# Optimization experiments

Measured on AMD Instinct MI355X. Metric: run time of the kernel, lower is better.

## Reference

```python
import jax, jax.numpy as jnp
import numpy as np

IN_DIM = 64
OUT_DIM = 64


def setup_inputs() -> dict:
    key = jax.random.key(0)
    k1, k2, k3, k4, k5, k6 = jax.random.split(key, 6)
    N, E = 50000, 800000
    features = jax.random.normal(k1, (N, IN_DIM), dtype=jnp.float32)
    src_idx = jax.random.randint(k2, (E,), 0, N, dtype=jnp.int64)
    # torch nn.Linear-style init (uniform +/- 1/sqrt(fan_in)); stored as [in, out]
    s1 = 1.0 / np.sqrt(IN_DIM)
    s2 = 1.0 / np.sqrt(OUT_DIM)
    W1 = jax.random.uniform(k3, (IN_DIM, OUT_DIM), jnp.float32, -s1, s1)
    b1 = jax.random.uniform(k4, (OUT_DIM,), jnp.float32, -s1, s1)
    W2 = jax.random.uniform(k5, (OUT_DIM, OUT_DIM), jnp.float32, -s2, s2)
    b2 = jax.random.uniform(k6, (OUT_DIM,), jnp.float32, -s2, s2)
    return {"features": features, "src_idx": src_idx, "W1": W1, "b1": b1, "W2": W2, "b2": b2}


def reference(features, src_idx, W1, b1, W2, b2):
    # gather source-node features per edge: [E, in_dim]
    x = features[src_idx]
    # Linear -> ReLU -> Linear -> ReLU
    h = jax.nn.relu(x @ W1 + b1)
    out = jax.nn.relu(h @ W2 + b2)  # [E, out_dim] == 'feature_n'
    return out
```

## Files before the change

kernel.cpp:

```cpp
#include <hip/hip_runtime.h>

typedef float f32x4 __attribute__((ext_vector_type(4)));
typedef _Float16 f16;
typedef f16 f16x8 __attribute__((ext_vector_type(8)));


__global__ __launch_bounds__(256) void cvt_kernel(
    const f32x4* __restrict__ in, f16x8* __restrict__ outv, int n8)
{
    const int stride = gridDim.x * blockDim.x;
    for (int i = blockIdx.x * blockDim.x + threadIdx.x; i < n8; i += stride) {
        const f32x4 a = in[2 * i];
        const f32x4 b = in[2 * i + 1];
        f16x8 o;
        #pragma unroll
        for (int j = 0; j < 4; ++j) { o[j] = (f16)a[j]; o[4 + j] = (f16)b[j]; }
        outv[i] = o;
    }
}

__global__ __launch_bounds__(256) void fused_mlp_kernel(
    const f16* __restrict__ feat16,
    const int* __restrict__ src,
    const float* __restrict__ W1, const float* __restrict__ b1,
    const float* __restrict__ W2, const float* __restrict__ b2,
    float* __restrict__ out, int E, int ntiles)
{
    __shared__ f16  hl[4][16][72];
    __shared__ float ol[4][16][68];

    const int lane = threadIdx.x & 63;
    const int wv   = threadIdx.x >> 6;
    const int l15  = lane & 15;
    const int q    = lane >> 4;

    const int gw = blockIdx.x * 4 + wv;
    const int nw = gridDim.x * 4;

    f16x8 B1f[4][2], B2f[4][2];
    #pragma unroll
    for (int t = 0; t < 4; ++t) {
        #pragma unroll
        for (int s = 0; s < 2; ++s) {
            f16x8 r1, r2;
            #pragma unroll
            for (int j = 0; j < 8; ++j) {
                const int kk = s * 32 + q * 8 + j;
                r1[j] = (f16)W1[kk * 64 + t * 16 + l15];
                r2[j] = (f16)W2[kk * 64 + t * 16 + l15];
            }
            B1f[t][s] = r1;
            B2f[t][s] = r2;
        }
    }
    float bb1[4], bb2[4];
    #pragma unroll
    for (int t = 0; t < 4; ++t) {
        bb1[t] = b1[t * 16 + l15];
        bb2[t] = b2[t * 16 + l15];
    }

    int tile = gw;
    if (tile >= ntiles) return;

    int er0 = tile * 16 + l15; if (er0 >= E) er0 = E - 1;
    int n = src[er0];
    const f16* fp0 = feat16 + (long long)n * 64;
    f16x8 A0 = *(const f16x8*)(fp0 + q * 8);
    f16x8 A1 = *(const f16x8*)(fp0 + 32 + q * 8);

    while (tile < ntiles) {
        const int e0 = tile * 16;
        const int tile_n = tile + nw;

        f16x8 nA0, nA1;
        if (tile_n < ntiles) {
            int er = tile_n * 16 + l15;
            if (er >= E) er = E - 1;
            const int nn = src[er];
            const f16* fp = feat16 + (long long)nn * 64;
            nA0 = *(const f16x8*)(fp + q * 8);
            nA1 = *(const f16x8*)(fp + 32 + q * 8);
        }

        f32x4 acc[4];
        #pragma unroll
        for (int t = 0; t < 4; ++t) acc[t] = (f32x4){bb1[t], bb1[t], bb1[t], bb1[t]};
        #pragma unroll
        for (int t = 0; t < 4; ++t) {
            acc[t] = __builtin_amdgcn_mfma_f32_16x16x32_f16(A0, B1f[t][0], acc[t], 0, 0, 0);
            acc[t] = __builtin_amdgcn_mfma_f32_16x16x32_f16(A1, B1f[t][1], acc[t], 0, 0, 0);
        }

        #pragma unroll
        for (int t = 0; t < 4; ++t)
            #pragma unroll
            for (int i = 0; i < 4; ++i)
                hl[wv][q * 4 + i][t * 16 + l15] = (f16)fmaxf(acc[t][i], 0.0f);

        const f16x8 A2a = *(const f16x8*)&hl[wv][l15][q * 8];
        const f16x8 A2b = *(const f16x8*)&hl[wv][l15][32 + q * 8];

        f32x4 acc2[4];
        #pragma unroll
        for (int t = 0; t < 4; ++t) acc2[t] = (f32x4){bb2[t], bb2[t], bb2[t], bb2[t]};
        #pragma unroll
        for (int t = 0; t < 4; ++t) {
            acc2[t] = __builtin_amdgcn_mfma_f32_16x16x32_f16(A2a, B2f[t][0], acc2[t], 0, 0, 0);
            acc2[t] = __builtin_amdgcn_mfma_f32_16x16x32_f16(A2b, B2f[t][1], acc2[t], 0, 0, 0);
        }

        if (e0 + 16 <= E) {
            #pragma unroll
            for (int t = 0; t < 4; ++t)
                #pragma unroll
                for (int i = 0; i < 4; ++i)
                    ol[wv][q * 4 + i][t * 16 + l15] = fmaxf(acc2[t][i], 0.0f);
            #pragma unroll
            for (int j = 0; j < 4; ++j) {
                const f32x4 v = *(const f32x4*)&ol[wv][4 * j + q][l15 * 4];
                __builtin_nontemporal_store(
                    v, (f32x4*)&out[(long long)(e0 + 4 * j + q) * 64 + l15 * 4]);
            }
        } else {
            #pragma unroll
            for (int t = 0; t < 4; ++t)
                #pragma unroll
                for (int i = 0; i < 4; ++i) {
                    const int row = e0 + q * 4 + i;
                    if (row < E)
                        __builtin_nontemporal_store(
                            fmaxf(acc2[t][i], 0.0f),
                            &out[(long long)row * 64 + t * 16 + l15]);
                }
        }

        A0 = nA0;
        A1 = nA1;
        tile = tile_n;
    }
}

__device__ __forceinline__ float bcast_f(float v, int l) {
    return __int_as_float(__builtin_amdgcn_readlane(__float_as_int(v), l));
}

__global__ __launch_bounds__(256, 3) void mlp_nodes_kernel(
    const float* __restrict__ features,
    const int* __restrict__ idx,
    const float* __restrict__ W1, const float* __restrict__ b1,
    const float* __restrict__ W2, const float* __restrict__ b2,
    float* __restrict__ out, int nrows)
{
    const int lane   = threadIdx.x & 63;
    const int wid    = (blockIdx.x * blockDim.x + threadIdx.x) >> 6;
    const int nwaves = (gridDim.x * blockDim.x) >> 6;

    float w1c[64], w2c[64];
    #pragma unroll
    for (int k = 0; k < 64; ++k) w1c[k] = W1[k * 64 + lane];
    #pragma unroll
    for (int k = 0; k < 64; ++k) w2c[k] = W2[k * 64 + lane];
    const float hb = b1[lane];
    const float yb = b2[lane];

    for (int row = wid; row < nrows; row += nwaves) {
        const int n = idx ? idx[row] : row;
        const float x = features[(long long)n * 64 + lane];
        float a0 = hb, a1 = 0.f, a2 = 0.f, a3 = 0.f;
        #pragma unroll
        for (int k = 0; k < 64; k += 4) {
            a0 = fmaf(bcast_f(x, k + 0), w1c[k + 0], a0);
            a1 = fmaf(bcast_f(x, k + 1), w1c[k + 1], a1);
            a2 = fmaf(bcast_f(x, k + 2), w1c[k + 2], a2);
            a3 = fmaf(bcast_f(x, k + 3), w1c[k + 3], a3);
        }
        const float h = fmaxf((a0 + a1) + (a2 + a3), 0.0f);
        float c0 = yb, c1 = 0.f, c2 = 0.f, c3 = 0.f;
        #pragma unroll
        for (int k = 0; k < 64; k += 4) {
            c0 = fmaf(bcast_f(h, k + 0), w2c[k + 0], c0);
            c1 = fmaf(bcast_f(h, k + 1), w2c[k + 1], c1);
            c2 = fmaf(bcast_f(h, k + 2), w2c[k + 2], c2);
            c3 = fmaf(bcast_f(h, k + 3), w2c[k + 3], c3);
        }
        out[(long long)row * 64 + lane] = fmaxf((c0 + c1) + (c2 + c3), 0.0f);
    }
}

extern "C" void kernel_launch(void* const* d_in, const int* in_sizes, int n_in,
                              void* d_out, int out_size, void* d_ws, size_t ws_size,
                              hipStream_t stream) {
    const float* features = (const float*)d_in[0];
    const int*   src      = (const int*)  d_in[1];
    const float* W1       = (const float*)d_in[2];
    const float* b1       = (const float*)d_in[3];
    const float* W2       = (const float*)d_in[4];
    const float* b2       = (const float*)d_in[5];
    float* out = (float*)d_out;

    const int N = in_sizes[0] / 64;
    const int E = in_sizes[1];

    const size_t need = (size_t)N * 64 * sizeof(f16);
    if (ws_size >= need) {
        f16* feat16 = (f16*)d_ws;
        cvt_kernel<<<1024, 256, 0, stream>>>(
            (const f32x4*)features, (f16x8*)feat16, N * 8);
        const int ntiles = (E + 15) / 16;
        fused_mlp_kernel<<<1024, 256, 0, stream>>>(
            feat16, src, W1, b1, W2, b2, out, E, ntiles);
    } else {
        mlp_nodes_kernel<<<3072, 256, 0, stream>>>(
            features, src, W1, b1, W2, b2, out, E);
    }
}
```

Before: 63.40 us.

## Deepen gather prefetch to two tiles ahead with double-buffered LDS staging

```diff
diff --git a/kernel.cpp b/kernel.cpp
--- a/kernel.cpp
+++ b/kernel.cpp
@@ -26,7 +26,7 @@
     const float* __restrict__ W2, const float* __restrict__ b2,
     float* __restrict__ out, int E, int ntiles)
 {
-    __shared__ f16  hl[4][16][72];
+    __shared__ f16   hl[2][4][16][72];
     __shared__ float ol[4][16][68];
 
     const int lane = threadIdx.x & 63;
@@ -60,28 +60,17 @@
         bb2[t] = b2[t * 16 + l15];
     }
 
-    int tile = gw;
-    if (tile >= ntiles) return;
-
-    int er0 = tile * 16 + l15; if (er0 >= E) er0 = E - 1;
-    int n = src[er0];
-    const f16* fp0 = feat16 + (long long)n * 64;
-    f16x8 A0 = *(const f16x8*)(fp0 + q * 8);
-    f16x8 A1 = *(const f16x8*)(fp0 + 32 + q * 8);
-
-    while (tile < ntiles) {
+    auto LOADFRAG = [&](int tile, f16x8& A0, f16x8& A1) {
+        int er = tile * 16 + l15;
+        if (er >= E) er = E - 1;
+        const int nn = src[er];
+        const f16* fp = feat16 + (long long)nn * 64;
+        A0 = *(const f16x8*)(fp + q * 8);
+        A1 = *(const f16x8*)(fp + 32 + q * 8);
+    };
+
+    auto COMPUTE = [&](int tile, int par, const f16x8& A0, const f16x8& A1) {
         const int e0 = tile * 16;
-        const int tile_n = tile + nw;
-
-        f16x8 nA0, nA1;
-        if (tile_n < ntiles) {
-            int er = tile_n * 16 + l15;
-            if (er >= E) er = E - 1;
-            const int nn = src[er];
-            const f16* fp = feat16 + (long long)nn * 64;
-            nA0 = *(const f16x8*)(fp + q * 8);
-            nA1 = *(const f16x8*)(fp + 32 + q * 8);
-        }
 
         f32x4 acc[4];
         #pragma unroll
@@ -96,10 +85,10 @@
         for (int t = 0; t < 4; ++t)
             #pragma unroll
             for (int i = 0; i < 4; ++i)
-                hl[wv][q * 4 + i][t * 16 + l15] = (f16)fmaxf(acc[t][i], 0.0f);
-
-        const f16x8 A2a = *(const f16x8*)&hl[wv][l15][q * 8];
-        const f16x8 A2b = *(const f16x8*)&hl[wv][l15][32 + q * 8];
+                hl[par][wv][q * 4 + i][t * 16 + l15] = (f16)fmaxf(acc[t][i], 0.0f);
+
+        const f16x8 A2a = *(const f16x8*)&hl[par][wv][l15][q * 8];
+        const f16x8 A2b = *(const f16x8*)&hl[par][wv][l15][32 + q * 8];
 
         f32x4 acc2[4];
         #pragma unroll
@@ -134,10 +123,30 @@
                             &out[(long long)row * 64 + t * 16 + l15]);
                 }
         }
-
-        A0 = nA0;
-        A1 = nA1;
-        tile = tile_n;
+    };
+
+    const int t0 = gw;
+    if (t0 >= ntiles) return;
+
+    f16x8 P0a, P0b, P1a, P1b, Ca, Cb, Da, Db;
+    LOADFRAG(t0, P0a, P0b);
+    {
+        const int tB = t0 + nw;
+        LOADFRAG(tB < ntiles ? tB : ntiles - 1, P1a, P1b);
+    }
+
+    const int step2 = 2 * nw;
+    for (int t = t0; t < ntiles; t += step2) {
+        const int tA = t, tB = t + nw;
+        const int tC = t + step2, tD = t + step2 + nw;
+
+        LOADFRAG(tC < ntiles ? tC : ntiles - 1, Ca, Cb);
+        COMPUTE(tA, 0, P0a, P0b);
+        LOADFRAG(tD < ntiles ? tD : ntiles - 1, Da, Db);
+        if (tB < ntiles) COMPUTE(tB, 1, P1a, P1b);
+
+        P0a = Ca; P0b = Cb;
+        P1a = Da; P1b = Db;
     }
 }
 
```

After: 54.79 us. 13.6% less time.
